# Kernel tuning notes

Hardware: AMD Instinct MI355X
Metric: run time of the kernel (lower is better)

## Reference

```python
import jax, jax.numpy as jnp
import numpy as np

LN_EPS = 1e-5   # torch nn.LayerNorm default
EPS = 1e-3      # module eps for norm denominator


def setup_inputs() -> dict:
    key = jax.random.key(0)
    ks = jax.random.split(key, 4)
    N_msa, N_tok, c_m, c_h, c_z = 64, 384, 64, 32, 128
    m = jax.random.normal(ks[0], (N_msa, N_tok, c_m), dtype=jnp.float32)
    mask = jnp.ones((N_msa, N_tok), dtype=jnp.float32)
    ln_w = jnp.ones((c_m,), dtype=jnp.float32)
    ln_b = jnp.zeros((c_m,), dtype=jnp.float32)
    w1 = jax.random.normal(ks[1], (c_h, c_m), dtype=jnp.float32) * (1.0 / np.sqrt(c_m))
    w2 = jax.random.normal(ks[2], (c_h, c_m), dtype=jnp.float32) * (1.0 / np.sqrt(c_m))
    w_out = jax.random.normal(ks[3], (c_z, c_h * c_h), dtype=jnp.float32) * (1.0 / np.sqrt(c_h * c_h))
    b_out = jnp.zeros((c_z,), dtype=jnp.float32)
    return {"m": m, "mask": mask, "ln_w": ln_w, "ln_b": ln_b,
            "w1": w1, "w2": w2, "w_out": w_out, "b_out": b_out}


def reference(m, mask, ln_w, ln_b, w1, w2, w_out, b_out):
    # LayerNorm over c_m
    mu = jnp.mean(m, axis=-1, keepdims=True)
    var = jnp.var(m, axis=-1, keepdims=True)
    m_n = (m - mu) * jax.lax.rsqrt(var + LN_EPS) * ln_w + ln_b

    maskx = mask[..., None]                                   # (N_msa, N_tok, 1)
    # norm[i,j] = sum_s mask[s,i]*mask[s,j], shape (N_tok, N_tok, 1)
    norm = jnp.einsum('sic,sjc->ijc', maskx, maskx)

    a = jnp.einsum('sim,cm->sic', m_n, w1) * maskx            # (N_msa, N_tok, C)
    b = jnp.einsum('sim,cm->sic', m_n, w2) * maskx            # (N_msa, N_tok, C)

    # mean-of-outer-products over MSA rows: (N_tok, N_tok, C, C)
    outer = jnp.einsum('sic,sjd->ijcd', a, b)
    N_tok, C = a.shape[1], a.shape[2]
    outer = outer.reshape(N_tok, N_tok, C * C)

    out = jnp.einsum('ijk,zk->ijz', outer, w_out) + b_out      # (N_tok, N_tok, c_z)
    return out / (norm + EPS)
```

## Files before the change

### kernel.cpp

```cpp
#include <hip/hip_runtime.h>
#include <stdint.h>

#define NS 64
#define NT 384
#define CM 64
#define CH 32
#define CZ 128

typedef __attribute__((ext_vector_type(8))) short bf16x8;
typedef __attribute__((ext_vector_type(16))) float f32x16;
typedef __attribute__((ext_vector_type(4))) float f32x4;

static __device__ __forceinline__ uint16_t f2bf(float f) {
  uint32_t u = __float_as_uint(f);
  u = (u + 0x7FFFu + ((u >> 16) & 1u)) >> 16;
  return (uint16_t)u;
}
static __device__ __forceinline__ uint32_t pack2(float lo, float hi) {
  return (uint32_t)f2bf(lo) | ((uint32_t)f2bf(hi) << 16);
}
static __device__ __forceinline__ int swz(int x) {
  return x ^ ((((x >> 7) ^ (x >> 11)) & 7) << 4);
}

__global__ __launch_bounds__(256) void k_prep(
    const float* __restrict__ m, const float* __restrict__ mask,
    const float* __restrict__ lnw, const float* __restrict__ lnb,
    const float* __restrict__ w1, const float* __restrict__ w2,
    uint16_t* __restrict__ AF, uint16_t* __restrict__ BF) {
  __shared__ float mn[64 * 65];
  __shared__ float wsh[2][64 * 64];
  const int i = blockIdx.x;
  const int tid = threadIdx.x;
  const int wv = tid >> 6, lane = tid & 63;

  for (int t = tid; t < 64 * 64; t += 256) {
    wsh[0][t] = w1[t];
    wsh[1][t] = w2[t];
  }

  const float lw = lnw[lane], lb = lnb[lane];
  for (int s = wv; s < NS; s += 4) {
    float x = m[(s * NT + i) * CM + lane];
    float sum = x, sq = x * x;
#pragma unroll
    for (int off = 32; off; off >>= 1) {
      sum += __shfl_xor(sum, off);
      sq  += __shfl_xor(sq, off);
    }
    float mu = sum * (1.f / 64.f);
    float var = sq * (1.f / 64.f) - mu * mu;
    float rs = 1.f / sqrtf(var + 1e-5f);
    mn[s * 65 + lane] = (x - mu) * rs * lw + lb;
  }
  __syncthreads();

  const int s = lane;
  const int cb = __builtin_amdgcn_readfirstlane(tid >> 6);
  float accA[8] = {0, 0, 0, 0, 0, 0, 0, 0};
  float accB[8] = {0, 0, 0, 0, 0, 0, 0, 0};
#pragma unroll 8
  for (int mm = 0; mm < CM; ++mm) {
    float v = mn[s * 65 + mm];
#pragma unroll
    for (int k = 0; k < 8; ++k) {
      accA[k] = fmaf(v, wsh[0][(cb * 8 + k) * CM + mm], accA[k]);
      accB[k] = fmaf(v, wsh[1][(cb * 8 + k) * CM + mm], accB[k]);
    }
  }
  const float msk = mask[s * NT + i];
  const int kkq = s >> 4, hh = (s >> 3) & 1, e = s & 7;
  const size_t base = ((size_t)(i * 4 + kkq) * 64 + hh * 32) * 8 + e;
#pragma unroll
  for (int k = 0; k < 8; ++k) {
    int c = cb * 8 + k;
    AF[base + c * 8] = f2bf(accA[k] * msk);
    BF[base + c * 8] = f2bf(accB[k] * msk);
  }
}

__global__ __launch_bounds__(256) void k_misc(
    const float* __restrict__ wout, const float* __restrict__ mask,
    uint16_t* __restrict__ W, float* __restrict__ invn) {
  const int b = blockIdx.x;
  if (b < 64) {
    const int g = b * 256 + threadIdx.x;
    const int l = g & 63, zt = (g >> 6) & 3, kk = g >> 8;
    const float* src = wout + (zt * 32 + (l & 31)) * 1024 + kk * 16 + (l >> 5) * 8;
    uint16_t* dst = W + (size_t)g * 8;
#pragma unroll
    for (int e = 0; e < 8; ++e) dst[e] = f2bf(src[e]);
  } else {
    const int t = (b - 64) * 256 + threadIdx.x;
    const int i = t / NT, j = t - i * NT;
    float acc = 0.f;
#pragma unroll 8
    for (int s = 0; s < NS; ++s) acc += mask[s * NT + i] * mask[s * NT + j];
    invn[t] = 1.f / (acc + 1e-3f);
  }
}

__global__ __launch_bounds__(512, 4) void k_main(
    const uint16_t* __restrict__ AF, const uint16_t* __restrict__ BF,
    const uint16_t* __restrict__ W, const float* __restrict__ b_out,
    const float* __restrict__ invn, float* __restrict__ out) {
  extern __shared__ char lds[];
  const int tid = threadIdx.x;
  const int wv = tid >> 6;
  const int l = tid & 63;
  const int lo5 = l & 31, hi = l >> 5;
  const int i0 = blockIdx.x * 8, j0 = blockIdx.y * 4;

  const int wm = wv >> 1, wn = wv & 1;
  f32x16 acc1[4];
#pragma unroll
  for (int r = 0; r < 4; ++r) acc1[r] = (f32x16){};

  const uint16_t* Abase = BF + ((size_t)(j0 + wm) * 4) * 512 + l * 8;
  const uint16_t* Bbase = AF + ((size_t)(i0 + wn * 4) * 4) * 512 + l * 8;
#pragma unroll
  for (int kk = 0; kk < 4; ++kk) {
    bf16x8 af = *(const bf16x8*)(Abase + kk * 512);
    bf16x8 bfr[4];
#pragma unroll
    for (int r = 0; r < 4; ++r) bfr[r] = *(const bf16x8*)(Bbase + (r * 4 + kk) * 512);
#pragma unroll
    for (int r = 0; r < 4; ++r)
      acc1[r] = __builtin_amdgcn_mfma_f32_32x32x16_bf16(af, bfr[r], acc1[r], 0, 0, 0);
  }

#pragma unroll
  for (int r = 0; r < 4; ++r) {
    const int p = wm * 8 + wn * 4 + r;
    const int base = p * 2048 + lo5 * 64 + hi * 8;
#pragma unroll
    for (int g = 0; g < 4; ++g) {
      uint64_t v = (uint64_t)pack2(acc1[r][4 * g + 0], acc1[r][4 * g + 1]) |
                   ((uint64_t)pack2(acc1[r][4 * g + 2], acc1[r][4 * g + 3]) << 32);
      *(uint64_t*)(lds + swz(base + g * 16)) = v;
    }
  }
  __syncthreads();

  const int wk = wv >> 2, wz = wv & 3;
  f32x16 acc2 = (f32x16){};
  const uint16_t* Wb = W + ((size_t)(wk * 32 * 4 + wz) * 64 + l) * 8;
  const int abyte0 = lo5 * 2048 + wk * 1024 + hi * 16;
#pragma unroll 8
  for (int kk = 0; kk < 32; ++kk) {
    bf16x8 a2 = *(const bf16x8*)(lds + swz(abyte0 + kk * 32));
    bf16x8 b2 = *(const bf16x8*)(Wb + (size_t)kk * 2048);
    acc2 = __builtin_amdgcn_mfma_f32_32x32x16_bf16(a2, b2, acc2, 0, 0, 0);
  }

  char* scr = lds + 65536;
  if (wk == 1) {
    const int sb = wz * 4096;
#pragma unroll
    for (int g = 0; g < 4; ++g) {
      f32x4 v = {acc2[4 * g + 0], acc2[4 * g + 1], acc2[4 * g + 2], acc2[4 * g + 3]};
      *(f32x4*)(scr + sb + ((l * 64 + g * 16) ^ ((l & 7) << 4))) = v;
    }
  }
  __syncthreads();
  if (wk == 0) {
    const int sb = wz * 4096;
#pragma unroll
    for (int g = 0; g < 4; ++g) {
      f32x4 v = *(const f32x4*)(scr + sb + ((l * 64 + g * 16) ^ ((l & 7) << 4)));
#pragma unroll
      for (int jj = 0; jj < 4; ++jj) acc2[4 * g + jj] += v[jj];
    }
    const int z = wz * 32 + lo5;
    const float bo = b_out[z];
#pragma unroll
    for (int e = 0; e < 16; ++e) {
      int p = (e & 3) + 8 * (e >> 2) + 4 * hi;
      int ti = p & 7, tj = p >> 3;
      int n = (i0 + ti) * NT + (j0 + tj);
      out[(size_t)n * CZ + z] = (acc2[e] + bo) * invn[n];
    }
  }
}

extern "C" void kernel_launch(void* const* d_in, const int* in_sizes, int n_in,
                              void* d_out, int out_size, void* d_ws, size_t ws_size,
                              hipStream_t stream) {
  const float* m    = (const float*)d_in[0];
  const float* mask = (const float*)d_in[1];
  const float* lnw  = (const float*)d_in[2];
  const float* lnb  = (const float*)d_in[3];
  const float* w1   = (const float*)d_in[4];
  const float* w2   = (const float*)d_in[5];
  const float* wout = (const float*)d_in[6];
  const float* bout = (const float*)d_in[7];
  float* out = (float*)d_out;

  char* ws = (char*)d_ws;
  uint16_t* AF  = (uint16_t*)ws;
  uint16_t* BF  = (uint16_t*)(ws + 1572864);
  uint16_t* W   = (uint16_t*)(ws + 3145728);
  float* invn   = (float*)(ws + 3407872);

  k_prep<<<NT, 256, 0, stream>>>(m, mask, lnw, lnb, w1, w2, AF, BF);
  k_misc<<<640, 256, 0, stream>>>(wout, mask, W, invn);

  (void)hipFuncSetAttribute(reinterpret_cast<const void*>(k_main),
                            hipFuncAttributeMaxDynamicSharedMemorySize, 81920);
  k_main<<<dim3(NT / 8, NT / 4), 512, 81920, stream>>>(AF, BF, W, bout, invn, out);
}
```

Baseline: 193.6 us.

## Enlarge main tile to 16x8 pairs, chunk outer-product over c-blocks with double-buffered W

The main kernel now handles a 16x8 token-pair tile per block and loops over eight c-blocks. Each c-block computes a slice of the outer product into LDS and stages the matching w_out slice in double-buffered LDS, so w_out is read once per larger tile rather than straight from global memory per wave. AF gets a new layout that matches this blocking. The two prep kernels are merged into one launch, and invn is cached in LDS for the epilogue. The cost is 128KB of LDS and lower occupancy (launch bound 2), plus a barrier per c-block.

```diff
diff --git a/kernel.cpp b/kernel.cpp
--- a/kernel.cpp
+++ b/kernel.cpp
@@ -10,6 +10,9 @@
 typedef __attribute__((ext_vector_type(8))) short bf16x8;
 typedef __attribute__((ext_vector_type(16))) float f32x16;
 typedef __attribute__((ext_vector_type(4))) float f32x4;
+typedef __attribute__((ext_vector_type(4))) uint32_t u32x4;
+
+#define MFMA __builtin_amdgcn_mfma_f32_32x32x16_bf16
 
 static __device__ __forceinline__ uint16_t f2bf(float f) {
   uint32_t u = __float_as_uint(f);
@@ -19,166 +22,220 @@
 static __device__ __forceinline__ uint32_t pack2(float lo, float hi) {
   return (uint32_t)f2bf(lo) | ((uint32_t)f2bf(hi) << 16);
 }
-static __device__ __forceinline__ int swz(int x) {
-  return x ^ ((((x >> 7) ^ (x >> 11)) & 7) << 4);
-}
-
-__global__ __launch_bounds__(256) void k_prep(
+static __device__ __forceinline__ int swzO(int x) {
+  return x ^ ((((x >> 8) ^ (x >> 11)) & 7) << 4);
+}
+
+__global__ __launch_bounds__(256) void k_pre(
     const float* __restrict__ m, const float* __restrict__ mask,
     const float* __restrict__ lnw, const float* __restrict__ lnb,
     const float* __restrict__ w1, const float* __restrict__ w2,
-    uint16_t* __restrict__ AF, uint16_t* __restrict__ BF) {
-  __shared__ float mn[64 * 65];
-  __shared__ float wsh[2][64 * 64];
-  const int i = blockIdx.x;
+    const float* __restrict__ wout,
+    uint16_t* __restrict__ AF2, uint16_t* __restrict__ BF,
+    uint16_t* __restrict__ W2, float* __restrict__ invn) {
+  __shared__ float4 wsh4[2][1024];
+  __shared__ float4 mn4[64 * 17];
+  const int b = blockIdx.x;
   const int tid = threadIdx.x;
-  const int wv = tid >> 6, lane = tid & 63;
-
-  for (int t = tid; t < 64 * 64; t += 256) {
-    wsh[0][t] = w1[t];
-    wsh[1][t] = w2[t];
-  }
-
-  const float lw = lnw[lane], lb = lnb[lane];
-  for (int s = wv; s < NS; s += 4) {
-    float x = m[(s * NT + i) * CM + lane];
-    float sum = x, sq = x * x;
-#pragma unroll
-    for (int off = 32; off; off >>= 1) {
-      sum += __shfl_xor(sum, off);
-      sq  += __shfl_xor(sq, off);
-    }
-    float mu = sum * (1.f / 64.f);
-    float var = sq * (1.f / 64.f) - mu * mu;
-    float rs = 1.f / sqrtf(var + 1e-5f);
-    mn[s * 65 + lane] = (x - mu) * rs * lw + lb;
-  }
-  __syncthreads();
-
-  const int s = lane;
-  const int cb = __builtin_amdgcn_readfirstlane(tid >> 6);
-  float accA[8] = {0, 0, 0, 0, 0, 0, 0, 0};
-  float accB[8] = {0, 0, 0, 0, 0, 0, 0, 0};
-#pragma unroll 8
-  for (int mm = 0; mm < CM; ++mm) {
-    float v = mn[s * 65 + mm];
+  if (b < NT) {
+    const int i = b;
+    const int wv = tid >> 6, lane = tid & 63;
+    for (int t = tid; t < 1024; t += 256) {
+      wsh4[0][t] = ((const float4*)w1)[t];
+      wsh4[1][t] = ((const float4*)w2)[t];
+    }
+    const float lw = lnw[lane], lb = lnb[lane];
+    float* mnf = (float*)mn4;
+    for (int s = wv; s < NS; s += 4) {
+      float x = m[(s * NT + i) * CM + lane];
+      float sum = x, sq = x * x;
+#pragma unroll
+      for (int off = 32; off; off >>= 1) {
+        sum += __shfl_xor(sum, off);
+        sq += __shfl_xor(sq, off);
+      }
+      float mu = sum * (1.f / 64.f);
+      float var = sq * (1.f / 64.f) - mu * mu;
+      float rs = 1.f / sqrtf(var + 1e-5f);
+      mnf[s * 68 + lane] = (x - mu) * rs * lw + lb;
+    }
+    __syncthreads();
+    const int s = lane;
+    const int cb = tid >> 6;
+    float accA[8] = {0, 0, 0, 0, 0, 0, 0, 0};
+    float accB[8] = {0, 0, 0, 0, 0, 0, 0, 0};
+#pragma unroll
+    for (int q = 0; q < 16; ++q) {
+      float4 v = mn4[s * 17 + q];
+#pragma unroll
+      for (int k = 0; k < 8; ++k) {
+        float4 wa = wsh4[0][(cb * 8 + k) * 16 + q];
+        float4 wb = wsh4[1][(cb * 8 + k) * 16 + q];
+        accA[k] = fmaf(v.x, wa.x, fmaf(v.y, wa.y, fmaf(v.z, wa.z, fmaf(v.w, wa.w, accA[k]))));
+        accB[k] = fmaf(v.x, wb.x, fmaf(v.y, wb.y, fmaf(v.z, wb.z, fmaf(v.w, wb.w, accB[k]))));
+      }
+    }
+    const float msk = mask[s * NT + i];
+    const int kkq = s >> 4, hh = (s >> 3) & 1, e = s & 7;
+    const size_t baseB = ((size_t)(i * 4 + kkq) * 64 + hh * 32) * 8 + e;
 #pragma unroll
     for (int k = 0; k < 8; ++k) {
-      accA[k] = fmaf(v, wsh[0][(cb * 8 + k) * CM + mm], accA[k]);
-      accB[k] = fmaf(v, wsh[1][(cb * 8 + k) * CM + mm], accB[k]);
-    }
-  }
-  const float msk = mask[s * NT + i];
-  const int kkq = s >> 4, hh = (s >> 3) & 1, e = s & 7;
-  const size_t base = ((size_t)(i * 4 + kkq) * 64 + hh * 32) * 8 + e;
-#pragma unroll
-  for (int k = 0; k < 8; ++k) {
-    int c = cb * 8 + k;
-    AF[base + c * 8] = f2bf(accA[k] * msk);
-    BF[base + c * 8] = f2bf(accB[k] * msk);
-  }
-}
-
-__global__ __launch_bounds__(256) void k_misc(
-    const float* __restrict__ wout, const float* __restrict__ mask,
-    uint16_t* __restrict__ W, float* __restrict__ invn) {
-  const int b = blockIdx.x;
-  if (b < 64) {
-    const int g = b * 256 + threadIdx.x;
+      int c = cb * 8 + k;
+      BF[baseB + (size_t)c * 8] = f2bf(accB[k] * msk);
+      int rb = (c >> 2) * 48 + (i >> 3);
+      int r = (i & 7) * 4 + (c & 3);
+      AF2[((size_t)(rb * 4 + kkq) * 64 + hh * 32 + r) * 8 + e] = f2bf(accA[k] * msk);
+    }
+  } else if (b < NT + 64) {
+    const int g = (b - NT) * 256 + tid;
     const int l = g & 63, zt = (g >> 6) & 3, kk = g >> 8;
     const float* src = wout + (zt * 32 + (l & 31)) * 1024 + kk * 16 + (l >> 5) * 8;
-    uint16_t* dst = W + (size_t)g * 8;
-#pragma unroll
-    for (int e = 0; e < 8; ++e) dst[e] = f2bf(src[e]);
+    uint16_t* dst = W2 + (size_t)g * 8;
+#pragma unroll
+    for (int e2 = 0; e2 < 8; ++e2) dst[e2] = f2bf(src[e2]);
   } else {
-    const int t = (b - 64) * 256 + threadIdx.x;
+    const int t = (b - NT - 64) * 256 + tid;
     const int i = t / NT, j = t - i * NT;
     float acc = 0.f;
 #pragma unroll 8
-    for (int s = 0; s < NS; ++s) acc += mask[s * NT + i] * mask[s * NT + j];
+    for (int s2 = 0; s2 < NS; ++s2) acc += mask[s2 * NT + i] * mask[s2 * NT + j];
     invn[t] = 1.f / (acc + 1e-3f);
   }
 }
 
-__global__ __launch_bounds__(512, 4) void k_main(
-    const uint16_t* __restrict__ AF, const uint16_t* __restrict__ BF,
-    const uint16_t* __restrict__ W, const float* __restrict__ b_out,
+__global__ __launch_bounds__(512, 2) void k_main(
+    const uint16_t* __restrict__ AF2, const uint16_t* __restrict__ BF,
+    const uint16_t* __restrict__ W2, const float* __restrict__ b_out,
     const float* __restrict__ invn, float* __restrict__ out) {
   extern __shared__ char lds[];
   const int tid = threadIdx.x;
-  const int wv = tid >> 6;
-  const int l = tid & 63;
+  const int wv = tid >> 6, l = tid & 63;
   const int lo5 = l & 31, hi = l >> 5;
-  const int i0 = blockIdx.x * 8, j0 = blockIdx.y * 4;
-
-  const int wm = wv >> 1, wn = wv & 1;
-  f32x16 acc1[4];
-#pragma unroll
-  for (int r = 0; r < 4; ++r) acc1[r] = (f32x16){};
-
-  const uint16_t* Abase = BF + ((size_t)(j0 + wm) * 4) * 512 + l * 8;
-  const uint16_t* Bbase = AF + ((size_t)(i0 + wn * 4) * 4) * 512 + l * 8;
-#pragma unroll
-  for (int kk = 0; kk < 4; ++kk) {
-    bf16x8 af = *(const bf16x8*)(Abase + kk * 512);
-    bf16x8 bfr[4];
-#pragma unroll
-    for (int r = 0; r < 4; ++r) bfr[r] = *(const bf16x8*)(Bbase + (r * 4 + kk) * 512);
-#pragma unroll
-    for (int r = 0; r < 4; ++r)
-      acc1[r] = __builtin_amdgcn_mfma_f32_32x32x16_bf16(af, bfr[r], acc1[r], 0, 0, 0);
-  }
-
-#pragma unroll
-  for (int r = 0; r < 4; ++r) {
-    const int p = wm * 8 + wn * 4 + r;
-    const int base = p * 2048 + lo5 * 64 + hi * 8;
-#pragma unroll
-    for (int g = 0; g < 4; ++g) {
-      uint64_t v = (uint64_t)pack2(acc1[r][4 * g + 0], acc1[r][4 * g + 1]) |
-                   ((uint64_t)pack2(acc1[r][4 * g + 2], acc1[r][4 * g + 3]) << 32);
-      *(uint64_t*)(lds + swz(base + g * 16)) = v;
-    }
+  const int i0 = blockIdx.x * 16, j0 = blockIdx.y * 8;
+  const int ib0 = blockIdx.x * 2;
+  const int jt = wv;
+  const int kh = wv >> 2, mp = (wv >> 1) & 1, zp = wv & 1;
+
+  bf16x8 bfr[4];
+  {
+    const uint16_t* p = BF + (size_t)(j0 + jt) * 4 * 512 + (size_t)l * 8;
+#pragma unroll
+    for (int kk = 0; kk < 4; ++kk) bfr[kk] = *(const bf16x8*)(p + kk * 512);
+  }
+
+  f32x16 acc2[2][2];
+#pragma unroll
+  for (int mi = 0; mi < 2; ++mi)
+#pragma unroll
+    for (int zi = 0; zi < 2; ++zi) acc2[mi][zi] = (f32x16){};
+
+  for (int cbk = 0; cbk < 8; ++cbk) {
+    const int cur = cbk & 1;
+    char* ldsO = lds + cur * 32768;
+    char* ldsW = lds + 65536 + cur * 32768;
+
+    u32x4 wst[4];
+    {
+      const uint32_t* src = (const uint32_t*)(W2 + (size_t)cbk * 16384);
+#pragma unroll
+      for (int it = 0; it < 4; ++it) wst[it] = *(const u32x4*)(src + it * 2048 + tid * 4);
+    }
+
+    f32x16 acc1[2];
+    acc1[0] = (f32x16){};
+    acc1[1] = (f32x16){};
+    {
+      const uint16_t* Ap = AF2 + (size_t)(cbk * 48 + ib0) * 4 * 512 + (size_t)l * 8;
+#pragma unroll
+      for (int kk = 0; kk < 4; ++kk) {
+        bf16x8 a0 = *(const bf16x8*)(Ap + kk * 512);
+        bf16x8 a1 = *(const bf16x8*)(Ap + (4 + kk) * 512);
+        acc1[0] = MFMA(bfr[kk], a0, acc1[0], 0, 0, 0);
+        acc1[1] = MFMA(bfr[kk], a1, acc1[1], 0, 0, 0);
+      }
+    }
+#pragma unroll
+    for (int it = 0; it < 4; ++it) *(u32x4*)(ldsW + it * 8192 + tid * 16) = wst[it];
+#pragma unroll
+    for (int h = 0; h < 2; ++h) {
+      const int p = (h * 8 + (lo5 >> 2)) * 8 + jt;
+      const int base = p * 256 + (lo5 & 3) * 64 + hi * 8;
+#pragma unroll
+      for (int g = 0; g < 4; ++g) {
+        uint64_t v = (uint64_t)pack2(acc1[h][4 * g + 0], acc1[h][4 * g + 1]) |
+                     ((uint64_t)pack2(acc1[h][4 * g + 2], acc1[h][4 * g + 3]) << 32);
+        *(uint64_t*)(ldsO + swzO(base + g * 16)) = v;
+      }
+    }
+    __syncthreads();
+
+#pragma unroll
+    for (int kx = 0; kx < 4; ++kx) {
+      const int kkl = kh * 4 + kx;
+      bf16x8 of[2], wf[2];
+#pragma unroll
+      for (int mi = 0; mi < 2; ++mi) {
+        const int mt = mp * 2 + mi;
+        of[mi] = *(const bf16x8*)(ldsO + swzO((mt * 32 + lo5) * 256 + kkl * 32 + hi * 16));
+      }
+#pragma unroll
+      for (int zi = 0; zi < 2; ++zi) {
+        const int zt = zp * 2 + zi;
+        wf[zi] = *(const bf16x8*)(ldsW + (kkl * 4 + zt) * 1024 + l * 16);
+      }
+#pragma unroll
+      for (int mi = 0; mi < 2; ++mi)
+#pragma unroll
+        for (int zi = 0; zi < 2; ++zi)
+          acc2[mi][zi] = MFMA(of[mi], wf[zi], acc2[mi][zi], 0, 0, 0);
+    }
+  }
+
+  const int sidx = mp * 2 + zp;
+  const int wbase = (sidx < 2) ? sidx * 16384 : 65536 + (sidx - 2) * 16384;
+  if (kh == 1) {
+#pragma unroll
+    for (int mi = 0; mi < 2; ++mi)
+#pragma unroll
+      for (int zi = 0; zi < 2; ++zi)
+#pragma unroll
+        for (int g = 0; g < 4; ++g) {
+          f32x4 v = {acc2[mi][zi][4 * g + 0], acc2[mi][zi][4 * g + 1],
+                     acc2[mi][zi][4 * g + 2], acc2[mi][zi][4 * g + 3]};
+          *(f32x4*)(lds + wbase + ((mi * 2 + zi) * 4 + g) * 1024 + l * 16) = v;
+        }
   }
   __syncthreads();
-
-  const int wk = wv >> 2, wz = wv & 3;
-  f32x16 acc2 = (f32x16){};
-  const uint16_t* Wb = W + ((size_t)(wk * 32 * 4 + wz) * 64 + l) * 8;
-  const int abyte0 = lo5 * 2048 + wk * 1024 + hi * 16;
-#pragma unroll 8
-  for (int kk = 0; kk < 32; ++kk) {
-    bf16x8 a2 = *(const bf16x8*)(lds + swz(abyte0 + kk * 32));
-    bf16x8 b2 = *(const bf16x8*)(Wb + (size_t)kk * 2048);
-    acc2 = __builtin_amdgcn_mfma_f32_32x32x16_bf16(a2, b2, acc2, 0, 0, 0);
-  }
-
-  char* scr = lds + 65536;
-  if (wk == 1) {
-    const int sb = wz * 4096;
-#pragma unroll
-    for (int g = 0; g < 4; ++g) {
-      f32x4 v = {acc2[4 * g + 0], acc2[4 * g + 1], acc2[4 * g + 2], acc2[4 * g + 3]};
-      *(f32x4*)(scr + sb + ((l * 64 + g * 16) ^ ((l & 7) << 4))) = v;
-    }
-  }
+  if (kh == 0) {
+#pragma unroll
+    for (int mi = 0; mi < 2; ++mi)
+#pragma unroll
+      for (int zi = 0; zi < 2; ++zi)
+#pragma unroll
+        for (int g = 0; g < 4; ++g) {
+          f32x4 v = *(const f32x4*)(lds + wbase + ((mi * 2 + zi) * 4 + g) * 1024 + l * 16);
+#pragma unroll
+          for (int jj = 0; jj < 4; ++jj) acc2[mi][zi][4 * g + jj] += v[jj];
+        }
+  }
+  if (tid < 128)
+    ((float*)(lds + 98304))[tid] = invn[(size_t)(i0 + (tid >> 3)) * NT + j0 + (tid & 7)];
   __syncthreads();
-  if (wk == 0) {
-    const int sb = wz * 4096;
-#pragma unroll
-    for (int g = 0; g < 4; ++g) {
-      f32x4 v = *(const f32x4*)(scr + sb + ((l * 64 + g * 16) ^ ((l & 7) << 4)));
-#pragma unroll
-      for (int jj = 0; jj < 4; ++jj) acc2[4 * g + jj] += v[jj];
-    }
-    const int z = wz * 32 + lo5;
-    const float bo = b_out[z];
-#pragma unroll
-    for (int e = 0; e < 16; ++e) {
-      int p = (e & 3) + 8 * (e >> 2) + 4 * hi;
-      int ti = p & 7, tj = p >> 3;
-      int n = (i0 + ti) * NT + (j0 + tj);
-      out[(size_t)n * CZ + z] = (acc2[e] + bo) * invn[n];
+  if (kh == 0) {
+    const float bo0 = b_out[(zp * 2) * 32 + lo5];
+    const float bo1 = b_out[(zp * 2 + 1) * 32 + lo5];
+    const float* invl = (const float*)(lds + 98304);
+#pragma unroll
+    for (int mi = 0; mi < 2; ++mi) {
+      const int mt = mp * 2 + mi;
+#pragma unroll
+      for (int e = 0; e < 16; ++e) {
+        const int row = mt * 32 + (e & 3) + 8 * (e >> 2) + 4 * hi;
+        const float inv = invl[row];
+        const size_t n = (size_t)(i0 + (row >> 3)) * NT + j0 + (row & 7);
+        out[n * CZ + zp * 64 + lo5] = (acc2[mi][0][e] + bo0) * inv;
+        out[n * CZ + zp * 64 + 32 + lo5] = (acc2[mi][1][e] + bo1) * inv;
+      }
     }
   }
 }
@@ -197,15 +254,14 @@
   float* out = (float*)d_out;
 
   char* ws = (char*)d_ws;
-  uint16_t* AF  = (uint16_t*)ws;
+  uint16_t* AF2 = (uint16_t*)ws;
   uint16_t* BF  = (uint16_t*)(ws + 1572864);
-  uint16_t* W   = (uint16_t*)(ws + 3145728);
+  uint16_t* W2  = (uint16_t*)(ws + 3145728);
   float* invn   = (float*)(ws + 3407872);
 
-  k_prep<<<NT, 256, 0, stream>>>(m, mask, lnw, lnb, w1, w2, AF, BF);
-  k_misc<<<640, 256, 0, stream>>>(wout, mask, W, invn);
+  k_pre<<<1024, 256, 0, stream>>>(m, mask, lnw, lnb, w1, w2, wout, AF2, BF, W2, invn);
 
   (void)hipFuncSetAttribute(reinterpret_cast<const void*>(k_main),
-                            hipFuncAttributeMaxDynamicSharedMemorySize, 81920);
-  k_main<<<dim3(NT / 8, NT / 4), 512, 81920, stream>>>(AF, BF, W, bout, invn, out);
-}
+                            hipFuncAttributeMaxDynamicSharedMemorySize, 131072);
+  k_main<<<dim3(NT / 16, NT / 8), 512, 131072, stream>>>(AF2, BF, W2, bout, invn, out);
+}
```

New measurement: 195.1 us. About the same (+0.8%).
